# Kernel optimization log

Measured on AMD Instinct MI355X. Metric: run time of the kernel, lower is better.

The kernel has to match this reference:

```python
import jax, jax.numpy as jnp
import numpy as np

B, C, H, W = 8, 2048, 14, 14
NUM_CLASSES, WORD_DIM, INTER_DIM = 80, 300, 1024


def setup_inputs() -> dict:
    key = jax.random.key(0)
    ks = jax.random.split(key, 8)
    s = 0.02
    return {
        "image_features": jax.random.normal(ks[0], (B, C, H, W), jnp.float32),
        "word_features": jax.random.normal(ks[1], (NUM_CLASSES, WORD_DIM), jnp.float32),
        "W1": jax.random.normal(ks[2], (INTER_DIM, C), jnp.float32) * s,
        "W2": jax.random.normal(ks[3], (INTER_DIM, WORD_DIM), jnp.float32) * s,
        "W3": jax.random.normal(ks[4], (INTER_DIM, INTER_DIM), jnp.float32) * s,
        "b3": jax.random.normal(ks[5], (INTER_DIM,), jnp.float32) * s,
        "Wa": jax.random.normal(ks[6], (1, INTER_DIM), jnp.float32) * s,
        "ba": jax.random.normal(ks[7], (1,), jnp.float32) * s,
        "num_classes": NUM_CLASSES,
    }


def reference(image_features, word_features, W1, W2, W3, b3, Wa, ba, num_classes):
    b, c, h, w = image_features.shape
    # [s, b, c] with s = h*w (spatial locations)
    img = image_features.reshape(b, c, h * w).transpose(2, 0, 1)
    f_wh = img @ W1.T                      # [s, b, D]
    f_wd = word_features @ W2.T            # [n, D]
    # additive-attention score MLP; broadcast to [s, b, n, D]
    lb = jnp.tanh(f_wh[:, :, None, :] * f_wd[None, None, :, :]) @ W3.T + b3
    coef = (lb @ Wa.T + ba)[..., 0]        # [s, b, n]
    coef = jax.nn.softmax(coef, axis=0)    # softmax over spatial locations
    # weighted sum over spatial dim -> [b, n, c]
    return jnp.einsum('sbc,sbn->bnc', img, coef)
```

## Files before the change

kernel.cpp:

```cpp
#include <hip/hip_runtime.h>
#include <math.h>

#define SB 196
#define SP 224
#define NB 8
#define NC 2048
#define ND 1024
#define NN 80
#define NW 300
#define CH 4
#define DCH (ND / CH)

typedef __bf16 v8bf __attribute__((ext_vector_type(8)));
typedef __bf16 v4bf __attribute__((ext_vector_type(4)));
typedef __bf16 v2bf __attribute__((ext_vector_type(2)));
typedef float  f32x4 __attribute__((ext_vector_type(4)));

__global__ __launch_bounds__(256) void k0_v(const float* __restrict__ W3,
                                            const float* __restrict__ Wa,
                                            float* __restrict__ v) {
    int d  = blockIdx.x * 256 + threadIdx.x;
    int e0 = blockIdx.y * 64;
    float p = 0.f;
    #pragma unroll 8
    for (int e = e0; e < e0 + 64; ++e) {
        p += Wa[e] * W3[(size_t)e * ND + d];
    }
    atomicAdd(&v[d], p);
}

__global__ __launch_bounds__(256) void k0_fwd(const float* __restrict__ word,
                                              const float* __restrict__ W2,
                                              const float* __restrict__ v,
                                              float2* __restrict__ wpack) {
    __shared__ __align__(16) float lword[NW];
    int n = blockIdx.x;
    int d = blockIdx.y * 256 + threadIdx.x;
    for (int i = threadIdx.x; i < NW; i += 256) lword[i] = word[(size_t)n * NW + i];
    __syncthreads();
    const float4* wr = (const float4*)(W2 + (size_t)d * NW);
    const float4* l4 = (const float4*)lword;
    float acc = 0.f;
    #pragma unroll 5
    for (int i = 0; i < NW / 4; ++i) {
        float4 a = wr[i], b = l4[i];
        acc += a.x * b.x + a.y * b.y + a.z * b.z + a.w * b.w;
    }
    float2 o;
    o.x = 2.8853900817779268f * acc;
    o.y = -2.f * v[d];
    wpack[(size_t)n * ND + d] = o;
}

__global__ __launch_bounds__(256) void kcast_w1(const float* __restrict__ W1,
                                                __bf16* __restrict__ O) {
    size_t i = ((size_t)blockIdx.x * 256 + threadIdx.x) * 4;
    float4 f = *(const float4*)(W1 + i);
    v4bf o;
    o[0] = (__bf16)f.x; o[1] = (__bf16)f.y; o[2] = (__bf16)f.z; o[3] = (__bf16)f.w;
    *(v4bf*)(O + i) = o;
}

__global__ __launch_bounds__(256) void kcast_x(const float* __restrict__ X,
                                               __bf16* __restrict__ Xt,
                                               __bf16* __restrict__ Xhi,
                                               __bf16* __restrict__ Xlo) {
    __shared__ float tile[64][65];
    const int b  = blockIdx.z;
    const int c0 = blockIdx.x * 64;
    const int s0 = blockIdx.y * 64;
    const int t  = threadIdx.x;
    const float* Xb = X + (size_t)b * NC * SB;
    {
        int ss = t & 63, cbase = t >> 6;
        #pragma unroll
        for (int r = 0; r < 16; ++r) {
            int cc = cbase + 4 * r;
            float val = (s0 + ss < SB) ? Xb[(size_t)(c0 + cc) * SB + s0 + ss] : 0.f;
            tile[cc][ss] = val;
        }
    }
    __syncthreads();
    {
        int cc = t & 63, sbase = t >> 6;
        #pragma unroll
        for (int r = 0; r < 16; ++r) {
            int ss = sbase + 4 * r;
            if (s0 + ss < SB)
                Xt[((size_t)b * SB + s0 + ss) * NC + c0 + cc] = (__bf16)tile[cc][ss];
        }
    }
    {
        int ss = t & 63, cbase = t >> 6;
        int sg = s0 + ss;
        #pragma unroll
        for (int r = 0; r < 16; ++r) {
            int cc = cbase + 4 * r;
            if (sg < SP) {
                float val = (sg < SB) ? tile[cc][ss] : 0.f;
                __bf16 h = (__bf16)val;
                __bf16 l = (__bf16)(val - (float)h);
                size_t base = ((size_t)b * NC + c0 + cc) * SP + sg;
                Xhi[base] = h;
                Xlo[base] = l;
            }
        }
    }
}

#define PITCH 40
__global__ __launch_bounds__(256) void k1_mfma(const __bf16* __restrict__ Xt,
                                               const __bf16* __restrict__ W1b,
                                               float* __restrict__ F) {
    __shared__ __align__(16) __bf16 lA[64 * PITCH];
    __shared__ __align__(16) __bf16 lB[64 * PITCH];
    const int t    = threadIdx.x;
    const int d0   = blockIdx.x * 64;
    const int s0   = blockIdx.y * 64;
    const int b    = blockIdx.z;
    const int lane = t & 63;
    const int wave = t >> 6;
    const int doff = (wave & 1) * 32;
    const int soff = (wave >> 1) * 32;
    const int quad = lane >> 4;
    const int l16  = lane & 15;

    f32x4 acc[2][2] = {};

    const int rr = t >> 2;
    const int cc = (t & 3) * 8;
    const bool sv = (s0 + rr) < SB;
    const __bf16* Ag = W1b + (size_t)(d0 + rr) * NC + cc;
    const __bf16* Bg = Xt + ((size_t)b * SB + (sv ? (s0 + rr) : 0)) * NC + cc;
    __bf16* lAw = lA + rr * PITCH + cc;
    __bf16* lBw = lB + rr * PITCH + cc;

    const __bf16* rA0 = lA + (doff + l16) * PITCH + quad * 8;
    const __bf16* rA1 = rA0 + 16 * PITCH;
    const __bf16* rB0 = lB + (soff + l16) * PITCH + quad * 8;
    const __bf16* rB1 = rB0 + 16 * PITCH;

    for (int k0 = 0; k0 < NC; k0 += 32) {
        uint4 a = *(const uint4*)(Ag + k0);
        uint4 bv = sv ? *(const uint4*)(Bg + k0) : make_uint4(0u, 0u, 0u, 0u);
        __syncthreads();
        *(uint4*)lAw = a;
        *(uint4*)lBw = bv;
        __syncthreads();
        v8bf a0 = *(const v8bf*)rA0;
        v8bf a1 = *(const v8bf*)rA1;
        v8bf b0 = *(const v8bf*)rB0;
        v8bf b1 = *(const v8bf*)rB1;
        acc[0][0] = __builtin_amdgcn_mfma_f32_16x16x32_bf16(a0, b0, acc[0][0], 0, 0, 0);
        acc[0][1] = __builtin_amdgcn_mfma_f32_16x16x32_bf16(a0, b1, acc[0][1], 0, 0, 0);
        acc[1][0] = __builtin_amdgcn_mfma_f32_16x16x32_bf16(a1, b0, acc[1][0], 0, 0, 0);
        acc[1][1] = __builtin_amdgcn_mfma_f32_16x16x32_bf16(a1, b1, acc[1][1], 0, 0, 0);
    }
    float* Fb = F + (size_t)b * ND * SB;
    #pragma unroll
    for (int i = 0; i < 2; ++i) {
        #pragma unroll
        for (int j = 0; j < 2; ++j) {
            int s = s0 + soff + j * 16 + l16;
            if (s < SB) {
                #pragma unroll
                for (int r = 0; r < 4; ++r) {
                    int d = d0 + doff + i * 16 + quad * 4 + r;
                    Fb[(size_t)d * SB + s] = acc[i][j][r];
                }
            }
        }
    }
}

__global__ __launch_bounds__(256) void k2a(const float* __restrict__ F,
                                           const float2* __restrict__ wpack,
                                           float* __restrict__ part) {
    const int n   = blockIdx.x;
    const int ch  = blockIdx.z;
    const int idx = blockIdx.y * 256 + threadIdx.x;
    const bool valid = idx < (NB * SB);
    const int iv = valid ? idx : 0;
    const int b  = iv / SB;
    const int s  = iv - b * SB;
    const float*  Fp  = F + ((size_t)b * ND + ch * DCH) * SB + s;
    const float4* wp4 = (const float4*)(wpack + (size_t)n * ND + ch * DCH);
    float acc = 0.f;
    #pragma unroll 4
    for (int d2 = 0; d2 < DCH / 2; ++d2) {
        float4 w = wp4[d2];
        float x0 = Fp[(size_t)(2 * d2)     * SB] * w.x;
        float x1 = Fp[(size_t)(2 * d2 + 1) * SB] * w.z;
        float e0 = __builtin_amdgcn_exp2f(x0);
        float e1 = __builtin_amdgcn_exp2f(x1);
        float r0 = __builtin_amdgcn_rcpf(1.f + e0);
        float r1 = __builtin_amdgcn_rcpf(1.f + e1);
        acc = fmaf(w.y, r0, acc);
        acc = fmaf(w.w, r1, acc);
    }
    if (valid)
        part[(((size_t)ch * NB + b) * NN + n) * 256 + s] = acc;
}

__global__ __launch_bounds__(256) void k2b(const float* __restrict__ part,
                                           __bf16* __restrict__ coefh,
                                           __bf16* __restrict__ coefl) {
    __shared__ float red[256];
    const int n = blockIdx.x;
    const int b = blockIdx.y;
    const int t = threadIdx.x;
    float acc = 0.f;
    #pragma unroll
    for (int ch = 0; ch < CH; ++ch)
        acc += part[(((size_t)ch * NB + b) * NN + n) * 256 + t];

    red[t] = (t < SB) ? acc : -1e30f;
    __syncthreads();
    #pragma unroll
    for (int off = 128; off > 0; off >>= 1) {
        if (t < off) red[t] = fmaxf(red[t], red[t + off]);
        __syncthreads();
    }
    float m = red[0];
    __syncthreads();
    float p = (t < SB) ? __expf(acc - m) : 0.f;
    red[t] = p;
    __syncthreads();
    #pragma unroll
    for (int off = 128; off > 0; off >>= 1) {
        if (t < off) red[t] += red[t + off];
        __syncthreads();
    }
    float inv = 1.f / red[0];
    if (t < SP) {
        float val = (t < SB) ? p * inv : 0.f;
        __bf16 h = (__bf16)val;
        __bf16 l = (__bf16)(val - (float)h);
        size_t base = ((size_t)b * NN + n) * SP + t;
        coefh[base] = h;
        coefl[base] = l;
    }
}

__global__ __launch_bounds__(256) void k3_mfma(const __bf16* __restrict__ Xhi,
                                               const __bf16* __restrict__ Xlo,
                                               const __bf16* __restrict__ coefh,
                                               const __bf16* __restrict__ coefl,
                                               float* __restrict__ out) {
    const int t     = threadIdx.x;
    const int wave  = t >> 6;
    const int lane  = t & 63;
    const int quad  = lane >> 4;
    const int l16   = lane & 15;
    const int b     = blockIdx.y;
    const int cbase = blockIdx.x * 64 + wave * 16;

    const __bf16* Bh = Xhi + ((size_t)b * NC + cbase + l16) * SP + quad * 8;
    const __bf16* Bl = Xlo + ((size_t)b * NC + cbase + l16) * SP + quad * 8;
    const __bf16* Ah = coefh + ((size_t)b * NN + l16) * SP + quad * 8;
    const __bf16* Al = coefl + ((size_t)b * NN + l16) * SP + quad * 8;

    f32x4 acc[5] = {};

    #pragma unroll
    for (int k0 = 0; k0 < SP; k0 += 32) {
        v8bf bh = *(const v8bf*)(Bh + k0);
        v8bf bl = *(const v8bf*)(Bl + k0);
        #pragma unroll
        for (int mt = 0; mt < 5; ++mt) {
            v8bf ah = *(const v8bf*)(Ah + (size_t)mt * 16 * SP + k0);
            v8bf al = *(const v8bf*)(Al + (size_t)mt * 16 * SP + k0);
            acc[mt] = __builtin_amdgcn_mfma_f32_16x16x32_bf16(ah, bh, acc[mt], 0, 0, 0);
            acc[mt] = __builtin_amdgcn_mfma_f32_16x16x32_bf16(al, bh, acc[mt], 0, 0, 0);
            acc[mt] = __builtin_amdgcn_mfma_f32_16x16x32_bf16(ah, bl, acc[mt], 0, 0, 0);
        }
    }
    #pragma unroll
    for (int mt = 0; mt < 5; ++mt) {
        #pragma unroll
        for (int r = 0; r < 4; ++r) {
            int n = mt * 16 + quad * 4 + r;
            out[((size_t)b * NN + n) * NC + cbase + l16] = acc[mt][r];
        }
    }
}

extern "C" void kernel_launch(void* const* d_in, const int* in_sizes, int n_in,
                              void* d_out, int out_size, void* d_ws, size_t ws_size,
                              hipStream_t stream) {
    const float* X    = (const float*)d_in[0];
    const float* word = (const float*)d_in[1];
    const float* W1   = (const float*)d_in[2];
    const float* W2   = (const float*)d_in[3];
    const float* W3   = (const float*)d_in[4];
    const float* Wa   = (const float*)d_in[6];
    float* out = (float*)d_out;

    char* ws = (char*)d_ws;
    float*  v     = (float*)ws;
    float2* wpack = (float2*)(v + ND);
    float*  part  = (float*)(wpack + (size_t)NN * ND);
    __bf16* coefh = (__bf16*)(part + (size_t)CH * NB * NN * 256);
    __bf16* coefl = coefh + (size_t)NB * NN * SP;
    __bf16* W1b   = coefl + (size_t)NB * NN * SP;
    __bf16* Xt    = W1b + (size_t)ND * NC;
    float*  F     = (float*)(Xt + (size_t)NB * SB * NC);
    __bf16* Xhi   = (__bf16*)(F + (size_t)NB * ND * SB);
    __bf16* Xlo   = Xhi + (size_t)NB * NC * SP;

    hipMemsetAsync(v, 0, ND * sizeof(float), stream);
    k0_v    <<<dim3(4, 16),                 256, 0, stream>>>(W3, Wa, v);
    k0_fwd  <<<dim3(NN, 4),                 256, 0, stream>>>(word, W2, v, wpack);
    kcast_w1<<<dim3((ND * NC) / (256 * 4)), 256, 0, stream>>>(W1, W1b);
    kcast_x <<<dim3(32, 4, NB),             256, 0, stream>>>(X, Xt, Xhi, Xlo);
    k1_mfma <<<dim3(16, 4, NB),             256, 0, stream>>>(Xt, W1b, F);
    k2a     <<<dim3(NN, 7, CH),             256, 0, stream>>>(F, wpack, part);
    k2b     <<<dim3(NN, NB),                256, 0, stream>>>(part, coefh, coefl);
    k3_mfma <<<dim3(NC / 64, NB),           256, 0, stream>>>(Xhi, Xlo, coefh, coefl, out);
}
```

Before: 192.5 us.

## Reuse F loads across four classes in k2a and fuse W1 cast into kcast_x

The score kernel now computes four classes per thread, so each loaded F value is reused four times instead of reloaded per class. The D-chunk count is doubled to keep enough blocks in flight. Separately, the W1 bf16 cast is folded into an extra z-slice of the transpose/cast kernel, removing one launch. The cost is more registers per thread, and since the kernel is heavy on exp and reciprocal work, the gain from fewer loads may be limited.

```diff
diff --git a/kernel.cpp b/kernel.cpp
--- a/kernel.cpp
+++ b/kernel.cpp
@@ -8,7 +8,7 @@
 #define ND 1024
 #define NN 80
 #define NW 300
-#define CH 4
+#define CH 8
 #define DCH (ND / CH)
 
 typedef __bf16 v8bf __attribute__((ext_vector_type(8)));
@@ -52,24 +52,30 @@
     wpack[(size_t)n * ND + d] = o;
 }
 
-__global__ __launch_bounds__(256) void kcast_w1(const float* __restrict__ W1,
-                                                __bf16* __restrict__ O) {
-    size_t i = ((size_t)blockIdx.x * 256 + threadIdx.x) * 4;
-    float4 f = *(const float4*)(W1 + i);
-    v4bf o;
-    o[0] = (__bf16)f.x; o[1] = (__bf16)f.y; o[2] = (__bf16)f.z; o[3] = (__bf16)f.w;
-    *(v4bf*)(O + i) = o;
-}
-
 __global__ __launch_bounds__(256) void kcast_x(const float* __restrict__ X,
+                                               const float* __restrict__ W1,
                                                __bf16* __restrict__ Xt,
                                                __bf16* __restrict__ Xhi,
-                                               __bf16* __restrict__ Xlo) {
+                                               __bf16* __restrict__ Xlo,
+                                               __bf16* __restrict__ W1b) {
+    const int t = threadIdx.x;
+    if (blockIdx.z == 8) {
+        unsigned int slice_tid = (blockIdx.x * 4 + blockIdx.y) * 256 + t;
+        #pragma unroll 4
+        for (int r = 0; r < 16; ++r) {
+            size_t i = ((size_t)slice_tid + (size_t)r * 32768) * 4;
+            float4 f = *(const float4*)(W1 + i);
+            v4bf o;
+            o[0] = (__bf16)f.x; o[1] = (__bf16)f.y;
+            o[2] = (__bf16)f.z; o[3] = (__bf16)f.w;
+            *(v4bf*)(W1b + i) = o;
+        }
+        return;
+    }
     __shared__ float tile[64][65];
     const int b  = blockIdx.z;
     const int c0 = blockIdx.x * 64;
     const int s0 = blockIdx.y * 64;
-    const int t  = threadIdx.x;
     const float* Xb = X + (size_t)b * NC * SB;
     {
         int ss = t & 63, cbase = t >> 6;
@@ -176,7 +182,7 @@
 __global__ __launch_bounds__(256) void k2a(const float* __restrict__ F,
                                            const float2* __restrict__ wpack,
                                            float* __restrict__ part) {
-    const int n   = blockIdx.x;
+    const int n0  = blockIdx.x * 4;
     const int ch  = blockIdx.z;
     const int idx = blockIdx.y * 256 + threadIdx.x;
     const bool valid = idx < (NB * SB);
@@ -184,22 +190,43 @@
     const int b  = iv / SB;
     const int s  = iv - b * SB;
     const float*  Fp  = F + ((size_t)b * ND + ch * DCH) * SB + s;
-    const float4* wp4 = (const float4*)(wpack + (size_t)n * ND + ch * DCH);
-    float acc = 0.f;
+    const float4* wp0 = (const float4*)(wpack + (size_t)(n0 + 0) * ND + ch * DCH);
+    const float4* wp1 = (const float4*)(wpack + (size_t)(n0 + 1) * ND + ch * DCH);
+    const float4* wp2 = (const float4*)(wpack + (size_t)(n0 + 2) * ND + ch * DCH);
+    const float4* wp3 = (const float4*)(wpack + (size_t)(n0 + 3) * ND + ch * DCH);
+    float a0 = 0.f, a1 = 0.f, a2 = 0.f, a3 = 0.f;
     #pragma unroll 4
     for (int d2 = 0; d2 < DCH / 2; ++d2) {
-        float4 w = wp4[d2];
-        float x0 = Fp[(size_t)(2 * d2)     * SB] * w.x;
-        float x1 = Fp[(size_t)(2 * d2 + 1) * SB] * w.z;
-        float e0 = __builtin_amdgcn_exp2f(x0);
-        float e1 = __builtin_amdgcn_exp2f(x1);
-        float r0 = __builtin_amdgcn_rcpf(1.f + e0);
-        float r1 = __builtin_amdgcn_rcpf(1.f + e1);
-        acc = fmaf(w.y, r0, acc);
-        acc = fmaf(w.w, r1, acc);
-    }
-    if (valid)
-        part[(((size_t)ch * NB + b) * NN + n) * 256 + s] = acc;
+        float f0 = Fp[(size_t)(2 * d2)     * SB];
+        float f1 = Fp[(size_t)(2 * d2 + 1) * SB];
+        float4 w0 = wp0[d2];
+        float4 w1 = wp1[d2];
+        float4 w2 = wp2[d2];
+        float4 w3 = wp3[d2];
+        float e00 = __builtin_amdgcn_exp2f(f0 * w0.x);
+        float e01 = __builtin_amdgcn_exp2f(f1 * w0.z);
+        float e10 = __builtin_amdgcn_exp2f(f0 * w1.x);
+        float e11 = __builtin_amdgcn_exp2f(f1 * w1.z);
+        float e20 = __builtin_amdgcn_exp2f(f0 * w2.x);
+        float e21 = __builtin_amdgcn_exp2f(f1 * w2.z);
+        float e30 = __builtin_amdgcn_exp2f(f0 * w3.x);
+        float e31 = __builtin_amdgcn_exp2f(f1 * w3.z);
+        a0 = fmaf(w0.y, __builtin_amdgcn_rcpf(1.f + e00), a0);
+        a0 = fmaf(w0.w, __builtin_amdgcn_rcpf(1.f + e01), a0);
+        a1 = fmaf(w1.y, __builtin_amdgcn_rcpf(1.f + e10), a1);
+        a1 = fmaf(w1.w, __builtin_amdgcn_rcpf(1.f + e11), a1);
+        a2 = fmaf(w2.y, __builtin_amdgcn_rcpf(1.f + e20), a2);
+        a2 = fmaf(w2.w, __builtin_amdgcn_rcpf(1.f + e21), a2);
+        a3 = fmaf(w3.y, __builtin_amdgcn_rcpf(1.f + e30), a3);
+        a3 = fmaf(w3.w, __builtin_amdgcn_rcpf(1.f + e31), a3);
+    }
+    if (valid) {
+        size_t base = ((size_t)ch * NB + b) * NN;
+        part[(base + n0 + 0) * 256 + s] = a0;
+        part[(base + n0 + 1) * 256 + s] = a1;
+        part[(base + n0 + 2) * 256 + s] = a2;
+        part[(base + n0 + 3) * 256 + s] = a3;
+    }
 }
 
 __global__ __launch_bounds__(256) void k2b(const float* __restrict__ part,
@@ -309,12 +336,11 @@
     __bf16* Xlo   = Xhi + (size_t)NB * NC * SP;
 
     hipMemsetAsync(v, 0, ND * sizeof(float), stream);
-    k0_v    <<<dim3(4, 16),                 256, 0, stream>>>(W3, Wa, v);
-    k0_fwd  <<<dim3(NN, 4),                 256, 0, stream>>>(word, W2, v, wpack);
-    kcast_w1<<<dim3((ND * NC) / (256 * 4)), 256, 0, stream>>>(W1, W1b);
-    kcast_x <<<dim3(32, 4, NB),             256, 0, stream>>>(X, Xt, Xhi, Xlo);
-    k1_mfma <<<dim3(16, 4, NB),             256, 0, stream>>>(Xt, W1b, F);
-    k2a     <<<dim3(NN, 7, CH),             256, 0, stream>>>(F, wpack, part);
-    k2b     <<<dim3(NN, NB),                256, 0, stream>>>(part, coefh, coefl);
-    k3_mfma <<<dim3(NC / 64, NB),           256, 0, stream>>>(Xhi, Xlo, coefh, coefl, out);
-}
+    k0_v   <<<dim3(4, 16),       256, 0, stream>>>(W3, Wa, v);
+    k0_fwd <<<dim3(NN, 4),       256, 0, stream>>>(word, W2, v, wpack);
+    kcast_x<<<dim3(32, 4, 9),    256, 0, stream>>>(X, W1, Xt, Xhi, Xlo, W1b);
+    k1_mfma<<<dim3(16, 4, NB),   256, 0, stream>>>(Xt, W1b, F);
+    k2a    <<<dim3(NN / 4, 7, CH), 256, 0, stream>>>(F, wpack, part);
+    k2b    <<<dim3(NN, NB),      256, 0, stream>>>(part, coefh, coefl);
+    k3_mfma<<<dim3(NC / 64, NB), 256, 0, stream>>>(Xhi, Xlo, coefh, coefl, out);
+}
```

After: 188.0 us. 2.3% less time.
